# Optimization experiments

Measured on AMD Instinct MI355X. Metric: run time of the kernel, lower is better.

Reference implementation:

```python
import jax, jax.numpy as jnp
import numpy as np

V = 32000; DM = 512; DS = 64; K = 4; INNER = 2048; KK = 3
B = 4; N = 512; LOOPS = 6; H_CYCLES = 2; POWER = 2


def _ln(x, g, b, eps=1e-5):
    mu = jnp.mean(x, -1, keepdims=True)
    var = jnp.mean(jnp.square(x - mu), -1, keepdims=True)
    return (x - mu) * jax.lax.rsqrt(var + eps) * g + b


def _sn(W, u):
    # torch spectral_norm: one power iteration (no grad through u,v), sigma differentiable through W
    v = W.T @ u
    v = v / (jnp.linalg.norm(v) + 1e-12)
    u2 = W @ v
    u2 = u2 / (jnp.linalg.norm(u2) + 1e-12)
    u2 = jax.lax.stop_gradient(u2)
    v = jax.lax.stop_gradient(v)
    sigma = u2 @ (W @ v)
    return W / sigma


def _block(Q_in, p):
    Qn = _ln(Q_in, p['g1'], p['b1'])                       # [B,N,d]
    qp = Qn.mean(1)                                        # [B,d]
    Wq = _sn(p['hqW'], p['uq'])
    Wk = _sn(p['hkW'], p['uk'])
    Oq = (qp @ Wq.T).reshape(-1, DM, DS)                   # [B,d,D]
    Ok = (qp @ Wk.T).reshape(-1, DM, DS)
    Pq = jax.nn.elu(jnp.einsum('bnd,bde->bne', Qn, Oq) + p['BQ']) + 1.0
    Pk = jax.nn.elu(jnp.einsum('bnd,bde->bne', Qn, Ok) + p['BK']) + 1.0
    Wm = jnp.maximum(jnp.einsum('bne,bme->bnm', Pq, Pk), 0.0) ** POWER  # [B,N,N]
    Att = jnp.einsum('bnm,bmd->bnd', Wm, Qn)
    Nrm = jnp.abs(Wm.sum(-1)) + 1.0                        # [B,N]
    m = Att / Nrm[..., None] - Qn
    mp = m @ p['mW'].T + p['mb']
    Qi = Q_in + jax.nn.softplus(p['dt']) * mp
    Qn2 = _ln(Qi, p['g2'], p['b2'])
    GU = Qn2 @ p['WupW'].T                                 # [B,N,2*inner]
    G, U = GU[..., :INNER], GU[..., INNER:]
    H = jax.nn.silu(G) * U
    Ht = jnp.transpose(H, (0, 2, 1))                       # [B,inner,N]
    Hc = jax.lax.conv_general_dilated(Ht, p['convW'], (1,), [(1, 1)],
                                      dimension_numbers=('NCH', 'OIH', 'NCH'),
                                      feature_group_count=INNER)
    Hc = jnp.transpose(Hc, (0, 2, 1))
    return Qi + Hc @ p['WdownW'].T


def _run(Q, bp):
    for i in range(K):
        Q = _block(Q, {k: v[i] for k, v in bp.items()})
    return Q


def setup_inputs() -> dict:
    key = jax.random.key(0)
    ks = iter(jax.random.split(key, 48))
    nrm = lambda s, std=0.02: jax.random.normal(next(ks), s, jnp.float32) * std
    inp = {}
    inp['inputs'] = jax.random.randint(next(ks), (B, N), 0, V, jnp.int32)
    inp['labels'] = jax.random.randint(next(ks), (B, N), 0, V, jnp.int32)
    inp['halted'] = jnp.ones((B,), bool)
    inp['steps'] = jnp.zeros((B,), jnp.int32)
    inp['carry_hidden'] = jnp.zeros((B, N, DM), jnp.float32)
    inp['carry_inputs'] = jnp.zeros((B, N), jnp.int32)
    inp['carry_labels'] = jnp.zeros((B, N), jnp.int32)
    inp['embedding'] = nrm((V, DM))
    inp['pos_emb'] = nrm((8192, DM))
    inp['in_g'] = jnp.ones((DM,), jnp.float32)
    inp['in_b'] = jnp.zeros((DM,), jnp.float32)
    inp['init_hidden'] = nrm((DM,))
    inp['dt'] = jnp.full((K,), 0.1, jnp.float32)
    inp['mW'] = nrm((K, DM, DM))
    inp['mb'] = jnp.zeros((K, DM), jnp.float32)
    inp['hqW'] = nrm((K, DM * DS, DM))
    inp['hkW'] = nrm((K, DM * DS, DM))
    uq = jax.random.normal(next(ks), (K, DM * DS), jnp.float32)
    uk = jax.random.normal(next(ks), (K, DM * DS), jnp.float32)
    inp['uq'] = uq / jnp.linalg.norm(uq, axis=-1, keepdims=True)
    inp['uk'] = uk / jnp.linalg.norm(uk, axis=-1, keepdims=True)
    inp['BQ'] = nrm((K, DS))
    inp['BK'] = nrm((K, DS))
    inp['g1'] = jnp.ones((K, DM), jnp.float32)
    inp['b1'] = jnp.zeros((K, DM), jnp.float32)
    inp['g2'] = jnp.ones((K, DM), jnp.float32)
    inp['b2'] = jnp.zeros((K, DM), jnp.float32)
    inp['WupW'] = nrm((K, 2 * INNER, DM))
    inp['convW'] = nrm((K, INNER, 1, KK))
    inp['WdownW'] = nrm((K, DM, INNER))
    inp['fin_g'] = jnp.ones((DM,), jnp.float32)
    inp['fin_b'] = jnp.zeros((DM,), jnp.float32)
    inp['halt_W'] = nrm((1, DM))
    inp['halt_b'] = jnp.full((1,), -5.0, jnp.float32)
    inp['lm_head'] = nrm((V, DM))
    return inp


def reference(inputs, labels, halted, steps, carry_hidden, carry_inputs, carry_labels,
              embedding, pos_emb, in_g, in_b, init_hidden, dt, mW, mb, hqW, hkW, uq, uk,
              BQ, BK, g1, b1, g2, b2, WupW, convW, WdownW, fin_g, fin_b, halt_W, halt_b, lm_head):
    bp = dict(dt=dt, mW=mW, mb=mb, hqW=hqW, hkW=hkW, uq=uq, uk=uk, BQ=BQ, BK=BK,
              g1=g1, b1=b1, g2=g2, b2=b2, WupW=WupW, convW=convW, WdownW=WdownW)
    new_hidden = jnp.where(halted[:, None, None], init_hidden, carry_hidden)
    new_steps = jnp.where(halted, jnp.zeros_like(steps), steps)
    new_inputs = jnp.where(halted[:, None], inputs, carry_inputs)
    X = _ln(embedding[new_inputs] + pos_emb[:inputs.shape[1]][None], in_g, in_b)
    Q = new_hidden
    for _ in range(H_CYCLES - 1):  # no_grad burn-in
        Q = jax.lax.stop_gradient(_run(Q + X, bp))
    Q = _run(Q + X, bp)            # gradient pass (L_cycles = 1)
    Qf = _ln(Q, fin_g, fin_b)
    logits = Qf @ lm_head.T
    halt_logits = Qf.mean(1) @ halt_W.T + halt_b
    new_steps = new_steps + 1
    new_halted = new_steps >= LOOPS
    return logits, halt_logits, jax.lax.stop_gradient(Q), new_steps, new_halted
```

## Files before the change

kernel.cpp:

```cpp
#include <hip/hip_runtime.h>
#include <stdint.h>

#define DMD 512
#define NSEQ 512
#define NBATCH 4
#define WROWS 32768
#define VOCAB 32000

#define OFF_HALT   65536000L
#define OFF_Q      65536004L
#define OFF_STEPS  66584580L
#define OFF_HALTED 66584584L

typedef __attribute__((ext_vector_type(8))) short short8v;
typedef __attribute__((ext_vector_type(4))) float f32x4;

__device__ __forceinline__ ushort f2bf(float f){
  uint u = __builtin_bit_cast(uint, f);
  u += 0x7fffu + ((u >> 16) & 1u);
  return (ushort)(u >> 16);
}
__device__ __forceinline__ float bf2f(ushort h){
  return __builtin_bit_cast(float, (uint)h << 16);
}

__device__ __forceinline__ float block_reduce_sum256(float v, float* red){
  int t = threadIdx.x;
  red[t] = v; __syncthreads();
  for (int o = 128; o; o >>= 1){
    if (t < o) red[t] += red[t+o];
    __syncthreads();
  }
  float r = red[0]; __syncthreads();
  return r;
}

template<int MODE, int TR, int QP, int HALT>
__global__ __launch_bounds__(512) void k_ln1(
    const float* in, float* QaW, const float* X,
    const int* halted32, const float* ih, const float* ch,
    ushort* __restrict__ outb, ushort* __restrict__ outT,
    float* __restrict__ qp_part,
    const float* __restrict__ g, const float* __restrict__ b,
    const float* __restrict__ hW, float* __restrict__ hpart)
{
  __shared__ ushort lt[TR ? 32 : 1][TR ? 514 : 1];
  __shared__ float red[QP ? 4096 : 1];
  const int bb = blockIdx.y, rg = blockIdx.x;
  const int n0 = rg*32;
  const int tid = threadIdx.x, wave = tid >> 6, lane = tid & 63;
  const int c8 = lane*8;
  float qacc[8] = {};
  #pragma unroll
  for (int rr = 0; rr < 4; rr++){
    const int n = n0 + wave*4 + rr;
    const long rowo = (long)bb*262144 + (long)n*512;
    float x[8];
    if (MODE == 1){
      bool hall = (halted32[0] != 0);
      #pragma unroll
      for (int i = 0; i < 8; i++){
        float base = hall ? ih[c8+i] : ch[rowo + c8 + i];
        x[i] = base + X[rowo + c8 + i];
      }
      #pragma unroll
      for (int i = 0; i < 8; i++) QaW[rowo + c8 + i] = x[i];
    } else if (MODE == 2){
      #pragma unroll
      for (int i = 0; i < 8; i++) x[i] = in[rowo + c8 + i] + X[rowo + c8 + i];
      #pragma unroll
      for (int i = 0; i < 8; i++) QaW[rowo + c8 + i] = x[i];
    } else {
      float4 a0 = *(const float4*)(in + rowo + c8);
      float4 a1 = *(const float4*)(in + rowo + c8 + 4);
      x[0]=a0.x; x[1]=a0.y; x[2]=a0.z; x[3]=a0.w;
      x[4]=a1.x; x[5]=a1.y; x[6]=a1.z; x[7]=a1.w;
    }
    float s = 0.f, sq = 0.f;
    #pragma unroll
    for (int i = 0; i < 8; i++){ s += x[i]; sq += x[i]*x[i]; }
    #pragma unroll
    for (int m = 32; m; m >>= 1){
      s  += __shfl_xor(s, m);
      sq += __shfl_xor(sq, m);
    }
    float mu = s*(1.f/512.f);
    float var = sq*(1.f/512.f) - mu*mu;
    float rs = rsqrtf(var + 1e-5f);
    float hd = 0.f;
    short8v ov;
    #pragma unroll
    for (int i = 0; i < 8; i++){
      float o = (x[i]-mu)*rs*g[c8+i] + b[c8+i];
      ov[i] = (short)f2bf(o);
      if (QP) qacc[i] += o;
      if (HALT) hd += o * hW[c8+i];
    }
    *(short8v*)&outb[rowo + c8] = ov;
    if (TR) *(short8v*)&lt[n & 31][c8] = ov;
    if (HALT){
      #pragma unroll
      for (int m = 32; m; m >>= 1) hd += __shfl_xor(hd, m);
      if (lane == 0) atomicAdd(&hpart[bb], hd);
    }
  }
  if (QP){
    #pragma unroll
    for (int i = 0; i < 8; i++) red[wave*512 + c8 + i] = qacc[i];
    __syncthreads();
    if (wave == 0){
      #pragma unroll
      for (int i = 0; i < 8; i++){
        int c = c8 + i;
        float s = 0.f;
        #pragma unroll
        for (int w = 0; w < 8; w++) s += red[w*512 + c];
        qp_part[((long)bb*16 + rg)*512 + c] = s;
      }
    }
  }
  if (TR){
    __syncthreads();
    #pragma unroll 4
    for (int p = 0; p < 32; p++){
      int d = p*16 + (tid >> 5);
      int n = tid & 31;
      outT[(long)bb*262144 + (long)d*512 + n0 + n] = lt[n][d];
    }
  }
}

__global__ void k_embed_ln(const int* __restrict__ inputs, const int* __restrict__ cinputs,
                           const int* __restrict__ halted32,
                           const float* __restrict__ emb, const float* __restrict__ pos,
                           const float* __restrict__ g, const float* __restrict__ b,
                           float* __restrict__ X){
  __shared__ float red[256];
  int r = blockIdx.x; int t = threadIdx.x;
  int n = r & 511;
  bool hall = (halted32[0] != 0);
  int tok = hall ? inputs[r] : cinputs[r];
  const float* e = emb + (long)tok*DMD;
  const float* p = pos + (long)n*DMD;
  float v0 = e[t]+p[t], v1 = e[t+256]+p[t+256];
  float mu = block_reduce_sum256(v0+v1, red) * (1.f/DMD);
  float d0 = v0-mu, d1 = v1-mu;
  float var = block_reduce_sum256(d0*d0+d1*d1, red) * (1.f/DMD);
  float rs = rsqrtf(var + 1e-5f);
  X[(long)r*DMD+t]     = d0*rs*g[t]     + b[t];
  X[(long)r*DMD+t+256] = d1*rs*g[t+256] + b[t+256];
}

__global__ __launch_bounds__(512) void k_sn_v(
    const float* __restrict__ hqW, const float* __restrict__ hkW,
    const float* __restrict__ uq, const float* __restrict__ uk,
    float* __restrict__ vraw, ushort* __restrict__ Wbf){
  __shared__ float red[4096];
  int z = blockIdx.y; int k = z >> 1, qk = z & 1;
  const float* W = (qk ? hkW : hqW) + (long)k*WROWS*DMD;
  const float* u = (qk ? uk : uq) + (long)k*WROWS;
  ushort* Wb = Wbf ? (Wbf + (long)z*WROWS*DMD) : nullptr;
  int t = threadIdx.x;
  int c8 = (t & 63) * 8;
  int rsub = t >> 6;
  int r0 = blockIdx.x * 256;
  float acc[8] = {};
  for (int r = rsub; r < 256; r += 8){
    int rr = r0 + r;
    long off = (long)rr*DMD + c8;
    float4 w0 = *(const float4*)(W + off);
    float4 w1 = *(const float4*)(W + off + 4);
    float uu = u[rr];
    float wv[8] = {w0.x,w0.y,w0.z,w0.w,w1.x,w1.y,w1.z,w1.w};
    #pragma unroll
    for (int i = 0; i < 8; i++) acc[i] += wv[i]*uu;
    if (Wb){
      short8v o;
      #pragma unroll
      for (int i = 0; i < 8; i++) o[i] = (short)f2bf(wv[i]);
      long colp = (long)((rr & 63)*512 + (rr >> 6));
      *(short8v*)(Wb + colp*DMD + c8) = o;
    }
  }
  #pragma unroll
  for (int i = 0; i < 8; i++) red[rsub*512 + c8 + i] = acc[i];
  __syncthreads();
  if (rsub == 0){
    #pragma unroll
    for (int i = 0; i < 8; i++){
      int c = c8 + i;
      float s = 0.f;
      #pragma unroll
      for (int w = 0; w < 8; w++) s += red[w*512 + c];
      atomicAdd(&vraw[z*DMD + c], s);
    }
  }
}

__global__ void k_sn_norm(float* __restrict__ vraw){
  __shared__ float red[512];
  int z = blockIdx.x; int t = threadIdx.x;
  float* v = vraw + z*DMD;
  float x = v[t];
  red[t] = x*x; __syncthreads();
  for (int o = 256; o; o >>= 1){
    if (t < o) red[t] += red[t+o];
    __syncthreads();
  }
  float nrm = sqrtf(red[0]);
  v[t] = x / (nrm + 1e-12f);
}

__global__ void k_vw(const float* __restrict__ vraw, ushort* __restrict__ qpb){
  int z = blockIdx.x, t = threadIdx.x;
  qpb[(long)z*32768 + 4*512 + t] = f2bf(vraw[z*512 + t]);
}

__global__ void k_sn_s(const float* __restrict__ hqW, const float* __restrict__ hkW,
                       const float* __restrict__ vraw, float* __restrict__ ssqp){
  int z = blockIdx.y; int k = z >> 1, qk = z & 1;
  const float* W = (qk ? hkW : hqW) + (long)k*WROWS*DMD;
  const float* v = vraw + z*DMD;
  int wave = threadIdx.x >> 6, lane = threadIdx.x & 63;
  float vreg[8];
  #pragma unroll
  for (int i = 0; i < 8; i++) vreg[i] = v[lane + 64*i];
  int r0 = blockIdx.x*256 + wave*64;
  float acc = 0.f;
  for (int r = r0; r < r0+64; r++){
    float p = 0.f;
    #pragma unroll
    for (int i = 0; i < 8; i++)
      p += W[(long)r*DMD + lane + 64*i] * vreg[i];
    for (int off = 32; off; off >>= 1) p += __shfl_down(p, off);
    if (lane == 0) acc += p*p;
  }
  if (lane == 0) atomicAdd(&ssqp[z*64 + (blockIdx.x & 63)], acc);
}

__global__ void k_proj(const float* __restrict__ hqW, const float* __restrict__ hkW,
                       const float* __restrict__ qp,
                       ushort* __restrict__ OqT, ushort* __restrict__ OkT, int k){
  int z = blockIdx.y;
  const float* W = (z ? hkW : hqW) + (long)k*WROWS*DMD;
  ushort* O = z ? OkT : OqT;
  int wave = threadIdx.x >> 6, lane = threadIdx.x & 63;
  long r = (long)blockIdx.x*4 + wave;
  float a0=0,a1=0,a2=0,a3=0;
  for (int j = lane; j < DMD; j += 64){
    float w = W[r*DMD + j];
    a0 += w*qp[j]; a1 += w*qp[DMD+j]; a2 += w*qp[2*DMD+j]; a3 += w*qp[3*DMD+j];
  }
  for (int off = 32; off; off >>= 1){
    a0 += __shfl_down(a0,off); a1 += __shfl_down(a1,off);
    a2 += __shfl_down(a2,off); a3 += __shfl_down(a3,off);
  }
  if (lane == 0){
    int d = (int)(r >> 6), e = (int)(r & 63);
    long o = (long)e*512 + d;
    O[o] = f2bf(a0); O[32768+o] = f2bf(a1);
    O[2*32768+o] = f2bf(a2); O[3*32768+o] = f2bf(a3);
  }
}

template<int BM, int BN, int WM, int WN, int EPI, int BFOUT, int DUAL, int RSUM>
__global__ __launch_bounds__(256) void mm_bt(
    const ushort* __restrict__ A, const ushort* __restrict__ B, void* __restrict__ C,
    int N, int K, long sA, long sB, long sC,
    const float* __restrict__ bias, const float* __restrict__ bias2,
    const float* __restrict__ res, const ushort* __restrict__ resb,
    const float* __restrict__ dtp, int dtidx,
    float* __restrict__ aux, const float* __restrict__ ssqp)
{
  __shared__ ushort As[BM*64];
  __shared__ ushort Bs[BN*64];
  const int z = blockIdx.z;
  const float* biasz = bias;
  if (DUAL){
    A += (long)(z & 3)*sA;
    if (z >= 4) biasz = bias2;
  } else {
    A += (long)z*sA;
  }
  B += (long)z*sB;
  const int tm = blockIdx.y*BM, tn = DUAL ? 0 : blockIdx.x*BN;
  const int tid = threadIdx.x;
  const int wid = tid >> 6, lane = tid & 63;
  constexpr int NWN = BN/WN;
  const int wr = wid / NWN, wc = wid % NWN;
  constexpr int FM = WM/16, FN = WN/16;
  const int ln15 = lane & 15, kq = lane >> 4;
  constexpr int LA = BM/32;
  constexpr int LB = BN/32;
  f32x4 acc[FM][FN] = {};

  for (int k0 = 0; k0 < K; k0 += 64){
    #pragma unroll
    for (int l = 0; l < LA; l++){
      int slot = tid + l*256;
      int row = slot >> 3, ch = slot & 7;
      int gch = ch ^ (row & 7);
      const char* g = (const char*)(A + (long)(tm+row)*K + k0) + gch*16;
      ushort* lp = As + (size_t)(wid*64 + l*256)*8;
      __builtin_amdgcn_global_load_lds((const __attribute__((address_space(1))) void*)g,
                                       (__attribute__((address_space(3))) void*)lp, 16, 0, 0);
    }
    #pragma unroll
    for (int l = 0; l < LB; l++){
      int slot = tid + l*256;
      int row = slot >> 3, ch = slot & 7;
      int gch = ch ^ (row & 7);
      const char* g = (const char*)(B + (long)(tn+row)*K + k0) + gch*16;
      ushort* lp = Bs + (size_t)(wid*64 + l*256)*8;
      __builtin_amdgcn_global_load_lds((const __attribute__((address_space(1))) void*)g,
                                       (__attribute__((address_space(3))) void*)lp, 16, 0, 0);
    }
    __syncthreads();
    #pragma unroll
    for (int ks = 0; ks < 2; ks++){
      short8v af[FM], bfr[FN];
      #pragma unroll
      for (int i = 0; i < FM; i++){
        int row = wr*WM + i*16 + ln15;
        af[i] = *(const short8v*)&As[row*64 + (((ks*4+kq) ^ (row&7))*8)];
      }
      #pragma unroll
      for (int j = 0; j < FN; j++){
        int row = wc*WN + j*16 + ln15;
        bfr[j] = *(const short8v*)&Bs[row*64 + (((ks*4+kq) ^ (row&7))*8)];
      }
      #pragma unroll
      for (int i = 0; i < FM; i++)
        #pragma unroll
        for (int j = 0; j < FN; j++)
          acc[i][j] = __builtin_amdgcn_mfma_f32_16x16x32_bf16(af[i], bfr[j], acc[i][j], 0, 0, 0);
    }
    __syncthreads();
  }

  float sp = 0.f, invs = 1.f;
  if (EPI == 3) sp = log1pf(expf(dtp[dtidx]));
  if (EPI == 1){
    const float* sq = ssqp + (DUAL ? (z >> 2)*64 : 0);
    float s2 = 0.f;
    for (int i = 0; i < 64; i++) s2 += sq[i];
    invs = (sqrtf(s2) + 1e-12f) / s2;
  }
  float* Cf = (float*)C + (long)z*sC;
  ushort* Cb = (ushort*)C + (long)z*sC;
  const float* rz = res ? (res + (long)z*sC) : nullptr;
  const ushort* rzb = resb ? (resb + (long)z*sC) : nullptr;
  const float* nrmz = (EPI == 5) ? (bias + (long)z*512) : nullptr;
  float rsv[FM][4] = {};
  float sacc = 0.f;
  #pragma unroll
  for (int i = 0; i < FM; i++){
    int row0 = tm + wr*WM + i*16 + kq*4;
    #pragma unroll
    for (int j = 0; j < FN; j++){
      int col = tn + wc*WN + j*16 + ln15;
      #pragma unroll
      for (int r = 0; r < 4; r++){
        int row = row0 + r;
        long idx = (long)row*N + col;
        float v = acc[i][j][r];
        if (EPI == 6){
          if (row < 4) Cb[idx] = f2bf(v);
          else if (row == 4) sacc += v*v;
          continue;
        }
        if (EPI == 1){ v = v*invs + biasz[col]; v = v > 0.f ? v : expm1f(v); v += 1.f; }
        else if (EPI == 2){ v = fmaxf(v, 0.f); v = v*v; if (RSUM) rsv[i][r] += v; }
        else if (EPI == 3){ v = rz[idx] + sp*(v + biasz[col]); }
        else if (EPI == 4){ v = v + rz[idx]; if (aux) aux[idx] = v; }
        else if (EPI == 5){ v = v/(fabsf(nrmz[row])+1.f) - bf2f(rzb[idx]); }
        if (BFOUT) Cb[idx] = f2bf(v);
        else       Cf[idx] = v;
      }
    }
  }
  if (EPI == 6){
    if (aux){
      sacc += __shfl_xor(sacc, 1); sacc += __shfl_xor(sacc, 2);
      sacc += __shfl_xor(sacc, 4); sacc += __shfl_xor(sacc, 8);
      if (wr == 0 && kq == 1 && ln15 == 0)
        atomicAdd(&aux[(long)z*64 + ((int)blockIdx.x & 63)], sacc);
    }
    return;
  }
  if (RSUM && EPI == 2){
    #pragma unroll
    for (int i = 0; i < FM; i++){
      #pragma unroll
      for (int r = 0; r < 4; r++){
        float x = rsv[i][r];
        x += __shfl_xor(x, 1); x += __shfl_xor(x, 2);
        x += __shfl_xor(x, 4); x += __shfl_xor(x, 8);
        if (ln15 == 0)
          atomicAdd(&aux[(long)z*512 + tm + wr*WM + i*16 + kq*4 + r], x);
      }
    }
  }
}

__global__ void k_qp2(const float* __restrict__ part, float* __restrict__ qp,
                      ushort* __restrict__ qpb, float* __restrict__ nrm_raw){
  int b = blockIdx.x, t = threadIdx.x;
  float s = 0.f;
  #pragma unroll
  for (int c = 0; c < 16; c++) s += part[((long)b*16 + c)*512 + t];
  float val = s * (1.f/512.f);
  qp[b*512 + t] = val;
  ushort bv = f2bf(val);
  #pragma unroll
  for (int z = 0; z < 8; z++)
    qpb[(long)z*32768 + (long)b*512 + t] = bv;
  nrm_raw[b*512 + t] = 0.f;
}

__global__ void k_convfuse(const ushort* __restrict__ GU, const float* __restrict__ w,
                           ushort* __restrict__ Hc){
  int r = blockIdx.x;
  int n = r & 511;
  int c = threadIdx.x * 8;
  long base = (long)r*4096 + c;
  float o[8] = {};
  if (n > 0){
    short8v gv = *(const short8v*)&GU[base-4096];
    short8v uv = *(const short8v*)&GU[base-4096+2048];
    #pragma unroll
    for (int i = 0; i < 8; i++){
      float g = bf2f((ushort)gv[i]), u = bf2f((ushort)uv[i]);
      o[i] += g/(1.f+expf(-g))*u * w[(c+i)*3+0];
    }
  }
  {
    short8v gv = *(const short8v*)&GU[base];
    short8v uv = *(const short8v*)&GU[base+2048];
    #pragma unroll
    for (int i = 0; i < 8; i++){
      float g = bf2f((ushort)gv[i]), u = bf2f((ushort)uv[i]);
      o[i] += g/(1.f+expf(-g))*u * w[(c+i)*3+1];
    }
  }
  if (n < 511){
    short8v gv = *(const short8v*)&GU[base+4096];
    short8v uv = *(const short8v*)&GU[base+4096+2048];
    #pragma unroll
    for (int i = 0; i < 8; i++){
      float g = bf2f((ushort)gv[i]), u = bf2f((ushort)uv[i]);
      o[i] += g/(1.f+expf(-g))*u * w[(c+i)*3+2];
    }
  }
  short8v ov;
  #pragma unroll
  for (int i = 0; i < 8; i++) ov[i] = (short)f2bf(o[i]);
  *(short8v*)&Hc[(long)r*2048 + c] = ov;
}

__global__ void k_cvt(const float* __restrict__ in, ushort* __restrict__ out){
  long i = ((long)blockIdx.x*256 + threadIdx.x)*4;
  float4 v = *(const float4*)(in + i);
  ushort4 o;
  o.x = f2bf(v.x); o.y = f2bf(v.y); o.z = f2bf(v.z); o.w = f2bf(v.w);
  *(ushort4*)(out + i) = o;
}

__global__ void k_fin(const int* __restrict__ halted32, const int* __restrict__ steps,
                      const float* __restrict__ hpart, const float* __restrict__ hb,
                      float* __restrict__ o_halt, float* __restrict__ o_steps,
                      float* __restrict__ o_halted){
  int t = threadIdx.x;
  if (t < NBATCH){
    o_halt[t] = hpart[t]*(1.f/512.f) + hb[0];
    bool hall = (halted32[0] != 0);
    int ns = (hall ? 0 : steps[t]) + 1;
    o_steps[t] = (float)ns;
    o_halted[t] = ns >= 6 ? 1.f : 0.f;
  }
}

extern "C" void kernel_launch(void* const* d_in, const int* in_sizes, int n_in,
                              void* d_out, int out_size, void* d_ws, size_t ws_size,
                              hipStream_t stream)
{
  const int*     inputs       = (const int*)d_in[0];
  const int*     halted32     = (const int*)d_in[2];
  const int*     steps        = (const int*)d_in[3];
  const float*   carry_hidden = (const float*)d_in[4];
  const int*     carry_inputs = (const int*)d_in[5];
  const float*   embedding    = (const float*)d_in[7];
  const float*   pos_emb      = (const float*)d_in[8];
  const float*   in_g = (const float*)d_in[9];
  const float*   in_b = (const float*)d_in[10];
  const float*   init_hidden = (const float*)d_in[11];
  const float*   dt   = (const float*)d_in[12];
  const float*   mW   = (const float*)d_in[13];
  const float*   mb   = (const float*)d_in[14];
  const float*   hqW  = (const float*)d_in[15];
  const float*   hkW  = (const float*)d_in[16];
  const float*   uq   = (const float*)d_in[17];
  const float*   uk   = (const float*)d_in[18];
  const float*   BQb  = (const float*)d_in[19];
  const float*   BKb  = (const float*)d_in[20];
  const float*   g1   = (const float*)d_in[21];
  const float*   b1   = (const float*)d_in[22];
  const float*   g2   = (const float*)d_in[23];
  const float*   b2   = (const float*)d_in[24];
  const float*   WupW = (const float*)d_in[25];
  const float*   convW= (const float*)d_in[26];
  const float*   WdownW=(const float*)d_in[27];
  const float*   fin_g= (const float*)d_in[28];
  const float*   fin_b= (const float*)d_in[29];
  const float*   halt_W=(const float*)d_in[30];
  const float*   halt_b=(const float*)d_in[31];
  const float*   lm_head=(const float*)d_in[32];
  float* out = (float*)d_out;

  float* ws = (float*)d_ws;
  float*  X    = ws;
  float*  Qa   = ws +  1048576;
  float*  Qb   = ws +  2097152;
  ushort* qpb  = (ushort*)(ws + 3145728);
  ushort* GU_bf  = (ushort*)(ws +  4194304);
  ushort* Hc_bf  = (ushort*)(ws +  8388608);
  ushort* m_bf   = (ushort*)(ws + 10485760);
  ushort* Wm_bf  = (ushort*)(ws + 11010048);
  ushort* QnT_bf = (ushort*)(ws + 11534336);
  ushort* Pq_bf  = (ushort*)(ws + 12058624);
  ushort* OqT    = (ushort*)(ws + 12189696);
  ushort* lm_bf  = (ushort*)(ws +  4194304);
  ushort* Qn_bf  = (ushort*)(ws + 13369344);
  ushort* mW_bf  = (ushort*)(ws + 13893632);
  ushort* Wup_bf = (ushort*)(ws + 14417920);
  ushort* Wdn_bf = (ushort*)(ws + 18612224);
  float*  qp       = ws + 20709376;
  float*  Nrm_raw  = ws + 20711424;
  float*  vraw     = ws + 20713472;
  float*  ssq_part = ws + 20717568;
  float*  hpart    = ws + 20718080;
  float*  qp_part  = ws + 20718144;
  ushort* W_bf = (ushort*)(ws + 20750976);
  const size_t NEED_BF = (size_t)(20750976 + 67108864) * 4;
  const bool useBf = ws_size >= NEED_BF;

  k_cvt<<<1024, 256, 0, stream>>>(mW, mW_bf);
  k_cvt<<<8192, 256, 0, stream>>>(WupW, Wup_bf);
  k_cvt<<<4096, 256, 0, stream>>>(WdownW, Wdn_bf);

  hipMemsetAsync(vraw, 0, 4672*sizeof(float), stream);
  hipMemsetAsync(qpb, 0, 8*64*512*sizeof(ushort), stream);
  k_sn_v<<<dim3(128,8), 512, 0, stream>>>(hqW, hkW, uq, uk, vraw,
                                          useBf ? W_bf : nullptr);
  k_sn_norm<<<8, 512, 0, stream>>>(vraw);
  k_vw<<<8, 512, 0, stream>>>(vraw, qpb);
  if (!useBf)
    k_sn_s<<<dim3(128,8), 256, 0, stream>>>(hqW, hkW, vraw, ssq_part);

  k_embed_ln<<<2048, 256, 0, stream>>>(inputs, carry_inputs, halted32,
                                       embedding, pos_emb, in_g, in_b, X);

  for (int cyc = 0; cyc < 2; cyc++){
    for (int k = 0; k < 4; k++){
      if (k == 0){
        if (cyc == 0)
          k_ln1<1,1,1,0><<<dim3(16,4), 512, 0, stream>>>(
              Qa, Qa, X, halted32, init_hidden, carry_hidden,
              Qn_bf, QnT_bf, qp_part, g1 + k*DMD, b1 + k*DMD, nullptr, nullptr);
        else
          k_ln1<2,1,1,0><<<dim3(16,4), 512, 0, stream>>>(
              Qa, Qa, X, nullptr, nullptr, nullptr,
              Qn_bf, QnT_bf, qp_part, g1 + k*DMD, b1 + k*DMD, nullptr, nullptr);
      } else {
        k_ln1<0,1,1,0><<<dim3(16,4), 512, 0, stream>>>(
            Qa, nullptr, nullptr, nullptr, nullptr, nullptr,
            Qn_bf, QnT_bf, qp_part, g1 + k*DMD, b1 + k*DMD, nullptr, nullptr);
      }
      k_qp2<<<4, 512, 0, stream>>>(qp_part, qp, qpb, Nrm_raw);
      if (useBf)
        mm_bt<64,64,32,32,6,1,0,1><<<dim3(512,1,2), 256, 0, stream>>>(
            qpb + (long)k*2*32768, W_bf + (long)k*2*16777216, OqT,
            32768, 512, 32768, 16777216, 131072,
            nullptr, nullptr, nullptr, nullptr, nullptr, 0,
            (cyc == 0) ? (ssq_part + k*128) : nullptr, nullptr);
      else
        k_proj<<<dim3(8192,2), 256, 0, stream>>>(hqW, hkW, qp, OqT, OqT + 131072, k);
      mm_bt<64,64,32,32,1,1,1,0><<<dim3(1,8,8), 256, 0, stream>>>(
          Qn_bf, OqT, Pq_bf, 64, 512, 262144, 32768, 32768,
          BQb + k*64, BKb + k*64, nullptr, nullptr, nullptr, 0,
          nullptr, ssq_part + k*128);
      mm_bt<64,64,32,32,2,1,0,1><<<dim3(8,8,4), 256, 0, stream>>>(
          Pq_bf, Pq_bf + 131072, Wm_bf, 512, 64, 32768, 32768, 262144,
          nullptr, nullptr, nullptr, nullptr, nullptr, 0, Nrm_raw, nullptr);
      mm_bt<64,64,32,32,5,1,0,0><<<dim3(8,8,4), 256, 0, stream>>>(
          Wm_bf, QnT_bf, m_bf, 512, 512, 262144, 262144, 262144,
          Nrm_raw, nullptr, nullptr, Qn_bf, nullptr, 0, nullptr, nullptr);
      mm_bt<64,64,32,32,3,0,0,0><<<dim3(8,32,1), 256, 0, stream>>>(
          m_bf, mW_bf + (long)k*262144, Qb, 512, 512, 0, 0, 0,
          mb + k*DMD, nullptr, Qa, nullptr, dt, k, nullptr, nullptr);
      k_ln1<0,0,0,0><<<dim3(16,4), 512, 0, stream>>>(
          Qb, nullptr, nullptr, nullptr, nullptr, nullptr,
          Qn_bf, nullptr, nullptr, g2 + k*DMD, b2 + k*DMD, nullptr, nullptr);
      mm_bt<128,128,64,64,0,1,0,0><<<dim3(32,16,1), 256, 0, stream>>>(
          Qn_bf, Wup_bf + (long)k*2097152, GU_bf, 4096, 512, 0, 0, 0,
          nullptr, nullptr, nullptr, nullptr, nullptr, 0, nullptr, nullptr);
      k_convfuse<<<2048, 256, 0, stream>>>(GU_bf, convW + (long)k*2048*3, Hc_bf);
      float* aux = (cyc == 1 && k == 3) ? (out + OFF_Q) : nullptr;
      mm_bt<64,64,32,32,4,0,0,0><<<dim3(8,32,1), 256, 0, stream>>>(
          Hc_bf, Wdn_bf + (long)k*1048576, Qa, 512, 2048, 0, 0, 0,
          nullptr, nullptr, Qb, nullptr, nullptr, 0, aux, nullptr);
    }
  }

  k_ln1<0,0,0,1><<<dim3(16,4), 512, 0, stream>>>(
      Qa, nullptr, nullptr, nullptr, nullptr, nullptr,
      Qn_bf, nullptr, nullptr, fin_g, fin_b, halt_W, hpart);
  k_cvt<<<16000, 256, 0, stream>>>(lm_head, lm_bf);
  mm_bt<128,128,64,64,0,0,0,0><<<dim3(250,16,1), 256, 0, stream>>>(
      Qn_bf, lm_bf, out, 32000, 512, 0, 0, 0,
      nullptr, nullptr, nullptr, nullptr, nullptr, 0, nullptr, nullptr);
  k_fin<<<1, 64, 0, stream>>>(halted32, steps, hpart, halt_b,
                              out + OFF_HALT, out + OFF_STEPS, out + OFF_HALTED);
}
```

Before: 1.582 ms.

## Merge weight conversions, replace atomics with partial sums, double LN grid

Three fp32-to-bf16 weight conversion launches become one combined kernel. The spectral-norm v reduction now writes per-block partial sums instead of using atomics, and the norm kernel folds in the final summation, the bf16 write and zeroing of the padded qpb rows, which removes one kernel and a memset. The layernorm kernel handles 16 rows per block instead of 32, doubling its grid from 64 to 128 blocks so more compute units are busy. The k_sn_v loop also processes two rows per iteration for more memory-level parallelism, and shared-memory strides are padded.

Measured after the change: 1.546 ms. -2.3%, faster.

```diff
diff --git a/kernel.cpp b/kernel.cpp
--- a/kernel.cpp
+++ b/kernel.cpp
@@ -44,16 +44,16 @@
     const float* __restrict__ g, const float* __restrict__ b,
     const float* __restrict__ hW, float* __restrict__ hpart)
 {
-  __shared__ ushort lt[TR ? 32 : 1][TR ? 514 : 1];
+  __shared__ ushort lt[TR ? 16 : 1][TR ? 520 : 1];
   __shared__ float red[QP ? 4096 : 1];
   const int bb = blockIdx.y, rg = blockIdx.x;
-  const int n0 = rg*32;
+  const int n0 = rg*16;
   const int tid = threadIdx.x, wave = tid >> 6, lane = tid & 63;
   const int c8 = lane*8;
   float qacc[8] = {};
   #pragma unroll
-  for (int rr = 0; rr < 4; rr++){
-    const int n = n0 + wave*4 + rr;
+  for (int rr = 0; rr < 2; rr++){
+    const int n = n0 + wave*2 + rr;
     const long rowo = (long)bb*262144 + (long)n*512;
     float x[8];
     if (MODE == 1){
@@ -97,7 +97,7 @@
       if (HALT) hd += o * hW[c8+i];
     }
     *(short8v*)&outb[rowo + c8] = ov;
-    if (TR) *(short8v*)&lt[n & 31][c8] = ov;
+    if (TR) *(short8v*)&lt[n & 15][c8] = ov;
     if (HALT){
       #pragma unroll
       for (int m = 32; m; m >>= 1) hd += __shfl_xor(hd, m);
@@ -115,16 +115,16 @@
         float s = 0.f;
         #pragma unroll
         for (int w = 0; w < 8; w++) s += red[w*512 + c];
-        qp_part[((long)bb*16 + rg)*512 + c] = s;
+        qp_part[((long)bb*32 + rg)*512 + c] = s;
       }
     }
   }
   if (TR){
     __syncthreads();
     #pragma unroll 4
-    for (int p = 0; p < 32; p++){
-      int d = p*16 + (tid >> 5);
-      int n = tid & 31;
+    for (int p = 0; p < 16; p++){
+      int d = p*32 + (tid >> 4);
+      int n = tid & 15;
       outT[(long)bb*262144 + (long)d*512 + n0 + n] = lt[n][d];
     }
   }
@@ -154,8 +154,8 @@
 __global__ __launch_bounds__(512) void k_sn_v(
     const float* __restrict__ hqW, const float* __restrict__ hkW,
     const float* __restrict__ uq, const float* __restrict__ uk,
-    float* __restrict__ vraw, ushort* __restrict__ Wbf){
-  __shared__ float red[4096];
+    float* __restrict__ vpart, ushort* __restrict__ Wbf){
+  __shared__ float red[8*520];
   int z = blockIdx.y; int k = z >> 1, qk = z & 1;
   const float* W = (qk ? hkW : hqW) + (long)k*WROWS*DMD;
   const float* u = (qk ? uk : uq) + (long)k*WROWS;
@@ -165,25 +165,30 @@
   int rsub = t >> 6;
   int r0 = blockIdx.x * 256;
   float acc[8] = {};
-  for (int r = rsub; r < 256; r += 8){
-    int rr = r0 + r;
-    long off = (long)rr*DMD + c8;
-    float4 w0 = *(const float4*)(W + off);
-    float4 w1 = *(const float4*)(W + off + 4);
-    float uu = u[rr];
-    float wv[8] = {w0.x,w0.y,w0.z,w0.w,w1.x,w1.y,w1.z,w1.w};
-    #pragma unroll
-    for (int i = 0; i < 8; i++) acc[i] += wv[i]*uu;
+  for (int r = rsub; r < 256; r += 16){
+    int ra = r0 + r, rb = r0 + r + 8;
+    long offa = (long)ra*DMD + c8, offb = (long)rb*DMD + c8;
+    float4 a0 = *(const float4*)(W + offa);
+    float4 a1 = *(const float4*)(W + offa + 4);
+    float4 b0 = *(const float4*)(W + offb);
+    float4 b1 = *(const float4*)(W + offb + 4);
+    float ua = u[ra], ub = u[rb];
+    float av[8] = {a0.x,a0.y,a0.z,a0.w,a1.x,a1.y,a1.z,a1.w};
+    float bv[8] = {b0.x,b0.y,b0.z,b0.w,b1.x,b1.y,b1.z,b1.w};
+    #pragma unroll
+    for (int i = 0; i < 8; i++) acc[i] += av[i]*ua + bv[i]*ub;
     if (Wb){
-      short8v o;
-      #pragma unroll
-      for (int i = 0; i < 8; i++) o[i] = (short)f2bf(wv[i]);
-      long colp = (long)((rr & 63)*512 + (rr >> 6));
-      *(short8v*)(Wb + colp*DMD + c8) = o;
+      short8v oa, ob;
+      #pragma unroll
+      for (int i = 0; i < 8; i++){ oa[i] = (short)f2bf(av[i]); ob[i] = (short)f2bf(bv[i]); }
+      long ca = (long)((ra & 63)*512 + (ra >> 6));
+      long cb = (long)((rb & 63)*512 + (rb >> 6));
+      *(short8v*)(Wb + ca*DMD + c8) = oa;
+      *(short8v*)(Wb + cb*DMD + c8) = ob;
     }
   }
   #pragma unroll
-  for (int i = 0; i < 8; i++) red[rsub*512 + c8 + i] = acc[i];
+  for (int i = 0; i < 8; i++) red[rsub*520 + c8 + i] = acc[i];
   __syncthreads();
   if (rsub == 0){
     #pragma unroll
@@ -191,29 +196,30 @@
       int c = c8 + i;
       float s = 0.f;
       #pragma unroll
-      for (int w = 0; w < 8; w++) s += red[w*512 + c];
-      atomicAdd(&vraw[z*DMD + c], s);
-    }
-  }
-}
-
-__global__ void k_sn_norm(float* __restrict__ vraw){
+      for (int w = 0; w < 8; w++) s += red[w*520 + c];
+      vpart[((long)z*128 + blockIdx.x)*512 + c] = s;
+    }
+  }
+}
+
+__global__ __launch_bounds__(512) void k_sn_norm(const float* __restrict__ vpart,
+                                                 float* __restrict__ vraw,
+                                                 ushort* __restrict__ qpb){
   __shared__ float red[512];
   int z = blockIdx.x; int t = threadIdx.x;
-  float* v = vraw + z*DMD;
-  float x = v[t];
-  red[t] = x*x; __syncthreads();
+  float s = 0.f;
+  for (int c = 0; c < 128; c++) s += vpart[((long)z*128 + c)*512 + t];
+  red[t] = s*s; __syncthreads();
   for (int o = 256; o; o >>= 1){
     if (t < o) red[t] += red[t+o];
     __syncthreads();
   }
   float nrm = sqrtf(red[0]);
-  v[t] = x / (nrm + 1e-12f);
-}
-
-__global__ void k_vw(const float* __restrict__ vraw, ushort* __restrict__ qpb){
-  int z = blockIdx.x, t = threadIdx.x;
-  qpb[(long)z*32768 + 4*512 + t] = f2bf(vraw[z*512 + t]);
+  float v = s / (nrm + 1e-12f);
+  vraw[z*512 + t] = v;
+  ushort* p = qpb + (long)z*32768;
+  p[4*512 + t] = f2bf(v);
+  for (int r = 5; r < 64; r++) p[r*512 + t] = 0;
 }
 
 __global__ void k_sn_s(const float* __restrict__ hqW, const float* __restrict__ hkW,
@@ -408,7 +414,7 @@
   int b = blockIdx.x, t = threadIdx.x;
   float s = 0.f;
   #pragma unroll
-  for (int c = 0; c < 16; c++) s += part[((long)b*16 + c)*512 + t];
+  for (int c = 0; c < 32; c++) s += part[((long)b*32 + c)*512 + t];
   float val = s * (1.f/512.f);
   qp[b*512 + t] = val;
   ushort bv = f2bf(val);
@@ -456,6 +462,20 @@
   #pragma unroll
   for (int i = 0; i < 8; i++) ov[i] = (short)f2bf(o[i]);
   *(short8v*)&Hc[(long)r*2048 + c] = ov;
+}
+
+__global__ void k_cvt3(const float* __restrict__ s0, ushort* __restrict__ d0, long n0,
+                       const float* __restrict__ s1, ushort* __restrict__ d1, long n1,
+                       const float* __restrict__ s2, ushort* __restrict__ d2, long n2){
+  long i = ((long)blockIdx.x*256 + threadIdx.x)*4;
+  const float* s; ushort* d; long off;
+  if (i < n0){ s = s0; d = d0; off = i; }
+  else if (i < n0 + n1){ s = s1; d = d1; off = i - n0; }
+  else { s = s2; d = d2; off = i - n0 - n1; }
+  float4 v = *(const float4*)(s + off);
+  ushort4 o;
+  o.x = f2bf(v.x); o.y = f2bf(v.y); o.z = f2bf(v.z); o.w = f2bf(v.w);
+  *(ushort4*)(d + off) = o;
 }
 
 __global__ void k_cvt(const float* __restrict__ in, ushort* __restrict__ out){
@@ -522,6 +542,8 @@
   float*  Qa   = ws +  1048576;
   float*  Qb   = ws +  2097152;
   ushort* qpb  = (ushort*)(ws + 3145728);
+  float*  vpart  = ws + 3276800;
+  float*  qp_part= ws + 3801088;
   ushort* GU_bf  = (ushort*)(ws +  4194304);
   ushort* Hc_bf  = (ushort*)(ws +  8388608);
   ushort* m_bf   = (ushort*)(ws + 10485760);
@@ -539,21 +561,18 @@
   float*  vraw     = ws + 20713472;
   float*  ssq_part = ws + 20717568;
   float*  hpart    = ws + 20718080;
-  float*  qp_part  = ws + 20718144;
   ushort* W_bf = (ushort*)(ws + 20750976);
   const size_t NEED_BF = (size_t)(20750976 + 67108864) * 4;
   const bool useBf = ws_size >= NEED_BF;
 
-  k_cvt<<<1024, 256, 0, stream>>>(mW, mW_bf);
-  k_cvt<<<8192, 256, 0, stream>>>(WupW, Wup_bf);
-  k_cvt<<<4096, 256, 0, stream>>>(WdownW, Wdn_bf);
-
-  hipMemsetAsync(vraw, 0, 4672*sizeof(float), stream);
-  hipMemsetAsync(qpb, 0, 8*64*512*sizeof(ushort), stream);
-  k_sn_v<<<dim3(128,8), 512, 0, stream>>>(hqW, hkW, uq, uk, vraw,
+  k_cvt3<<<13312, 256, 0, stream>>>(mW, mW_bf, 1048576L,
+                                    WupW, Wup_bf, 8388608L,
+                                    WdownW, Wdn_bf, 4194304L);
+
+  hipMemsetAsync(ssq_part, 0, 576*sizeof(float), stream);
+  k_sn_v<<<dim3(128,8), 512, 0, stream>>>(hqW, hkW, uq, uk, vpart,
                                           useBf ? W_bf : nullptr);
-  k_sn_norm<<<8, 512, 0, stream>>>(vraw);
-  k_vw<<<8, 512, 0, stream>>>(vraw, qpb);
+  k_sn_norm<<<8, 512, 0, stream>>>(vpart, vraw, qpb);
   if (!useBf)
     k_sn_s<<<dim3(128,8), 256, 0, stream>>>(hqW, hkW, vraw, ssq_part);
 
@@ -564,15 +583,15 @@
     for (int k = 0; k < 4; k++){
       if (k == 0){
         if (cyc == 0)
-          k_ln1<1,1,1,0><<<dim3(16,4), 512, 0, stream>>>(
+          k_ln1<1,1,1,0><<<dim3(32,4), 512, 0, stream>>>(
               Qa, Qa, X, halted32, init_hidden, carry_hidden,
               Qn_bf, QnT_bf, qp_part, g1 + k*DMD, b1 + k*DMD, nullptr, nullptr);
         else
-          k_ln1<2,1,1,0><<<dim3(16,4), 512, 0, stream>>>(
+          k_ln1<2,1,1,0><<<dim3(32,4), 512, 0, stream>>>(
               Qa, Qa, X, nullptr, nullptr, nullptr,
               Qn_bf, QnT_bf, qp_part, g1 + k*DMD, b1 + k*DMD, nullptr, nullptr);
       } else {
-        k_ln1<0,1,1,0><<<dim3(16,4), 512, 0, stream>>>(
+        k_ln1<0,1,1,0><<<dim3(32,4), 512, 0, stream>>>(
             Qa, nullptr, nullptr, nullptr, nullptr, nullptr,
             Qn_bf, QnT_bf, qp_part, g1 + k*DMD, b1 + k*DMD, nullptr, nullptr);
       }
@@ -598,7 +617,7 @@
       mm_bt<64,64,32,32,3,0,0,0><<<dim3(8,32,1), 256, 0, stream>>>(
           m_bf, mW_bf + (long)k*262144, Qb, 512, 512, 0, 0, 0,
           mb + k*DMD, nullptr, Qa, nullptr, dt, k, nullptr, nullptr);
-      k_ln1<0,0,0,0><<<dim3(16,4), 512, 0, stream>>>(
+      k_ln1<0,0,0,0><<<dim3(32,4), 512, 0, stream>>>(
           Qb, nullptr, nullptr, nullptr, nullptr, nullptr,
           Qn_bf, nullptr, nullptr, g2 + k*DMD, b2 + k*DMD, nullptr, nullptr);
       mm_bt<128,128,64,64,0,1,0,0><<<dim3(32,16,1), 256, 0, stream>>>(
@@ -612,7 +631,7 @@
     }
   }
 
-  k_ln1<0,0,0,1><<<dim3(16,4), 512, 0, stream>>>(
+  k_ln1<0,0,0,1><<<dim3(32,4), 512, 0, stream>>>(
       Qa, nullptr, nullptr, nullptr, nullptr, nullptr,
       Qn_bf, nullptr, nullptr, fin_g, fin_b, halt_W, hpart);
   k_cvt<<<16000, 256, 0, stream>>>(lm_head, lm_bf);
```
